# Kernel optimization log

Measured on AMD Instinct MI355X. Metric: run time of the kernel, lower is better.

The kernel has to match this reference:

```python
import jax, jax.numpy as jnp
import numpy as np

D_MODEL = 1024
N_HEADS = 16
N_PHASE = 128
HEAD_DIM = D_MODEL // N_HEADS
PHASE_PER_HEAD = N_PHASE // N_HEADS
CONTENT_SCALE = 1.0 / np.sqrt(HEAD_DIM)
PHASE_SCALE = 1.0 / np.sqrt(PHASE_PER_HEAD)
LN_EPS = 1e-5


def create_position_phases(L, n_phase, base=10000.0):
    # RoPE-style: each freq repeated at even/odd indices (interleaved)
    inv_freq = 1.0 / base ** (jnp.arange(0, n_phase, 2, dtype=jnp.float32) / n_phase)
    pos = jnp.arange(L, dtype=jnp.float32)
    sinusoid = pos[:, None] * inv_freq[None, :]          # (L, n_phase//2)
    return jnp.repeat(sinusoid, 2, axis=1)               # (L, n_phase)


def setup_inputs() -> dict:
    key = jax.random.key(0)
    ks = jax.random.split(key, 12)
    B, L, D, P = 1, 2048, D_MODEL, N_PHASE
    s = 0.02
    return {
        'x_real': jax.random.normal(ks[0], (B, L, D), jnp.float32),
        'x_imag': jax.random.normal(ks[1], (B, L, D), jnp.float32),
        'Wq': jax.random.normal(ks[2], (D, D), jnp.float32) * s,
        'Wk': jax.random.normal(ks[3], (D, D), jnp.float32) * s,
        'Wv': jax.random.normal(ks[4], (D, D), jnp.float32) * s,
        'Wqp': jax.random.normal(ks[5], (D, P), jnp.float32) * s,
        'bqp': jax.random.uniform(ks[6], (P,), jnp.float32, -np.pi, np.pi),
        'Wkp': jax.random.normal(ks[7], (D, P), jnp.float32) * s,
        'bkp': jax.random.uniform(ks[8], (P,), jnp.float32, -np.pi, np.pi),
        'Wo': jax.random.normal(ks[9], (D, D), jnp.float32) * s,
        'alpha_logit': jnp.zeros((N_HEADS, 1, 1), jnp.float32),
        'ln_gamma': jnp.ones((D,), jnp.float32),
        'ln_beta': jnp.zeros((D,), jnp.float32),
    }


def _split_heads(x, B, L, H, hd):
    return x.reshape(B, L, H, hd).transpose(0, 2, 1, 3)  # (B,H,L,hd)


def reference(x_real, x_imag, Wq, Wk, Wv, Wqp, bqp, Wkp, bkp, Wo,
              alpha_logit, ln_gamma, ln_beta):
    B, L, D = x_real.shape
    H, hd, p = N_HEADS, HEAD_DIM, PHASE_PER_HEAD

    Q = _split_heads(x_real @ Wq, B, L, H, hd)
    K = _split_heads(x_real @ Wk, B, L, H, hd)
    V = _split_heads(x_real @ Wv, B, L, H, hd)
    content = jnp.einsum('bhqd,bhkd->bhqk', Q, K) * CONTENT_SCALE

    pos_phase = create_position_phases(L, N_PHASE)        # (L, P)
    Qt = _split_heads(x_imag @ Wqp + bqp + pos_phase, B, L, H, p)
    Kt = _split_heads(x_imag @ Wkp + bkp + pos_phase, B, L, H, p)
    phase = (jnp.einsum('bhqp,bhkp->bhqk', jnp.cos(Qt), jnp.cos(Kt))
             + jnp.einsum('bhqp,bhkp->bhqk', jnp.sin(Qt), jnp.sin(Kt))) * PHASE_SCALE

    alpha = jax.nn.sigmoid(alpha_logit)                   # (H,1,1) broadcasts over (B,H,L,L)
    scores = (1.0 - alpha) * content + alpha * phase

    causal = jnp.triu(jnp.ones((L, L), bool), 1)
    scores = jnp.where(causal, -jnp.inf, scores)
    attn = jax.nn.softmax(scores, axis=-1)

    out = jnp.einsum('bhqk,bhkd->bhqd', attn, V)
    out = out.transpose(0, 2, 1, 3).reshape(B, L, D) @ Wo

    h = x_real + out
    mu = jnp.mean(h, axis=-1, keepdims=True)
    var = jnp.var(h, axis=-1, keepdims=True)
    out_real = (h - mu) / jnp.sqrt(var + LN_EPS) * ln_gamma + ln_beta
    return out_real, x_imag
```

## Files before the change

kernel.cpp:

```cpp
#include <hip/hip_runtime.h>
#include <hip/hip_bf16.h>
#include <math.h>

#define L 2048
#define D 1024
#define NH 16
#define HD 64
#define P 128
#define HDE 96
#define CONTENT_SCALE 0.125f
#define PHASE_SCALE   0.35355339059327373f
#define VTS 72
#define PLS 72
#define NSPLIT 4

typedef short bf16x8 __attribute__((ext_vector_type(8)));
typedef float f32x4 __attribute__((ext_vector_type(4)));

__device__ inline ushort f2b(float x) {
    __hip_bfloat16 b = __float2bfloat16(x);
    return *(ushort*)&b;
}
__device__ inline float b2f(ushort u) {
    unsigned v = (unsigned)u << 16;
    union { unsigned u; float f; } c; c.u = v; return c.f;
}

__device__ inline void sincos_hw(float ang, float* sn, float* cs) {
    float rev = ang * 0.15915494309189535f;
    rev -= floorf(rev);
    *sn = __builtin_amdgcn_sinf(rev);
    *cs = __builtin_amdgcn_cosf(rev);
}

__device__ inline void gld_lds16(const void* g, void* l) {
    __builtin_amdgcn_global_load_lds(
        (const __attribute__((address_space(1))) unsigned int*)g,
        (__attribute__((address_space(3))) unsigned int*)l,
        16, 0, 0);
}

__global__ void cvt2_kernel(const float4* __restrict__ sa, const float4* __restrict__ sb,
                            ushort4* __restrict__ da, ushort4* __restrict__ db, int n4) {
    const float4* src = blockIdx.y ? sb : sa;
    ushort4* dst = blockIdx.y ? db : da;
    int i = blockIdx.x * blockDim.x + threadIdx.x;
    if (i < n4) {
        float4 v = src[i];
        ushort4 o;
        o.x = f2b(v.x); o.y = f2b(v.y); o.z = f2b(v.z); o.w = f2b(v.w);
        dst[i] = o;
    }
}

__global__ void cvtw_kernel(const float* __restrict__ W0, const float* __restrict__ W1,
                            const float* __restrict__ W2, const float* __restrict__ W3,
                            const float* __restrict__ W4, const float* __restrict__ W5,
                            ushort* __restrict__ T0, ushort* __restrict__ T1,
                            ushort* __restrict__ T2, ushort* __restrict__ T3,
                            ushort* __restrict__ Tp) {
    const float* W; ushort* T; int ncols;
    switch (blockIdx.z) {
        case 0: W = W0; T = T0; ncols = D; break;
        case 1: W = W1; T = T1; ncols = D; break;
        case 2: W = W2; T = T2; ncols = D; break;
        case 3: W = W3; T = T3; ncols = D; break;
        case 4: W = W4; T = Tp; ncols = P; break;
        default: W = W5; T = Tp + (size_t)P * D; ncols = P; break;
    }
    int n0 = blockIdx.x * 32, k0 = blockIdx.y * 32;
    if (n0 >= ncols) return;
    __shared__ float tile[32][33];
    int tx = threadIdx.x, ty = threadIdx.y;
#pragma unroll
    for (int i = 0; i < 4; i++)
        tile[ty + i * 8][tx] = W[(size_t)(k0 + ty + i * 8) * ncols + n0 + tx];
    __syncthreads();
#pragma unroll
    for (int i = 0; i < 4; i++)
        T[(size_t)(n0 + ty + i * 8) * D + k0 + tx] = f2b(tile[tx][ty + i * 8]);
}

__global__ void zpad_kernel(ushort* __restrict__ Qe, ushort* __restrict__ Ke) {
    int i = blockIdx.x * blockDim.x + threadIdx.x;
    size_t base = (size_t)i * HDE + 80;
    uint4 z = make_uint4(0, 0, 0, 0);
    *(uint4*)(Qe + base) = z;
    *(uint4*)(Qe + base + 8) = z;
    *(uint4*)(Ke + base) = z;
    *(uint4*)(Ke + base + 8) = z;
}

__launch_bounds__(256)
__global__ void qkv_gemm(const ushort* __restrict__ Ab, const ushort* __restrict__ xib,
                         const ushort* __restrict__ Wtq, const ushort* __restrict__ Wtk,
                         const ushort* __restrict__ Wtv, const ushort* __restrict__ Wtp,
                         ushort* __restrict__ Qe, ushort* __restrict__ Ke,
                         ushort* __restrict__ Ve, const float* __restrict__ alpha,
                         const float* __restrict__ bqp, const float* __restrict__ bkp) {
    const int z = blockIdx.z;
    if (z == 3 && blockIdx.x >= 2) return;
    const ushort* At = (z == 3) ? xib : Ab;
    const ushort* Bt = (z == 0) ? Wtq : ((z == 1) ? Wtk : ((z == 2) ? Wtv : Wtp));
    __shared__ ushort As[128 * 32];
    __shared__ ushort Bs[128 * 32];
    const int tid = threadIdx.x;
    const int wave = tid >> 6, lane = tid & 63, quad = lane >> 4, ln16 = lane & 15;
    const int wm = wave >> 1, wn = wave & 1;
    const int m0 = blockIdx.y * 128, n0 = blockIdx.x * 128;
    f32x4 acc[4][4];
#pragma unroll
    for (int i = 0; i < 4; i++)
#pragma unroll
        for (int j = 0; j < 4; j++) acc[i][j] = (f32x4){0.f, 0.f, 0.f, 0.f};
    for (int kt = 0; kt < D; kt += 32) {
        __syncthreads();
#pragma unroll
        for (int i = 0; i < 2; i++) {
            int idx = i * 256 + tid;
            int row = idx >> 2, c8 = idx & 3;
            gld_lds16(At + (size_t)(m0 + row) * D + kt + c8 * 8, &As[idx * 8]);
            gld_lds16(Bt + (size_t)(n0 + row) * D + kt + c8 * 8, &Bs[idx * 8]);
        }
        __syncthreads();
        bf16x8 af[4], bfr[4];
#pragma unroll
        for (int t = 0; t < 4; t++) {
            af[t]  = *(const bf16x8*)(&As[(wm * 64 + t * 16 + ln16) * 32 + quad * 8]);
            bfr[t] = *(const bf16x8*)(&Bs[(wn * 64 + t * 16 + ln16) * 32 + quad * 8]);
        }
#pragma unroll
        for (int i = 0; i < 4; i++)
#pragma unroll
            for (int j = 0; j < 4; j++)
                acc[i][j] = __builtin_amdgcn_mfma_f32_16x16x32_bf16(af[i], bfr[j], acc[i][j], 0, 0, 0);
    }
    if (z < 3) {
        int hn = (n0 + wn * 64) >> 6;
        float s = 1.f;
        if (z == 0) s = (1.f - 1.f / (1.f + __expf(-alpha[hn]))) * CONTENT_SCALE;
        ushort* dst; int stride;
        if (z == 0)      { dst = Qe; stride = HDE; }
        else if (z == 1) { dst = Ke; stride = HDE; }
        else             { dst = Ve; stride = HD; }
#pragma unroll
        for (int i = 0; i < 4; i++)
#pragma unroll
            for (int j = 0; j < 4; j++) {
                int dcol = j * 16 + ln16;
#pragma unroll
                for (int r = 0; r < 4; r++) {
                    int m = m0 + wm * 64 + i * 16 + quad * 4 + r;
                    dst[((size_t)hn * L + m) * stride + dcol] = f2b(acc[i][j][r] * s);
                }
            }
    } else {
#pragma unroll
        for (int j = 0; j < 4; j++) {
            int cg = n0 + wn * 64 + j * 16 + ln16;
            int isQ = cg < P;
            int c = cg & (P - 1);
            int hh = c >> 3, jj = c & 7;
            float b = isQ ? bqp[c] : bkp[c];
            float sc = isQ ? (1.f / (1.f + __expf(-alpha[hh]))) * PHASE_SCALE : 1.f;
            float invf = __expf(-((float)(c & ~1) / 128.f) * 9.210340371976184f);
            ushort* dst = isQ ? Qe : Ke;
#pragma unroll
            for (int i = 0; i < 4; i++)
#pragma unroll
                for (int r = 0; r < 4; r++) {
                    int m = m0 + wm * 64 + i * 16 + quad * 4 + r;
                    float qt = acc[i][j][r] + b + (float)m * invf;
                    float sn, cs;
                    sincos_hw(qt, &sn, &cs);
                    size_t base = ((size_t)hh * L + m) * HDE;
                    dst[base + 64 + jj] = f2b(sc * cs);
                    dst[base + 72 + jj] = f2b(sc * sn);
                }
        }
    }
}

__launch_bounds__(256)
__global__ void wo_gemm(const ushort* __restrict__ Ab, const ushort* __restrict__ Bt,
                        float* __restrict__ C) {
    __shared__ ushort As[128 * 32];
    __shared__ ushort Bs[128 * 32];
    const int tid = threadIdx.x;
    const int wave = tid >> 6, lane = tid & 63, quad = lane >> 4, ln16 = lane & 15;
    const int wm = wave >> 1, wn = wave & 1;
    const int m0 = blockIdx.y * 128, n0 = blockIdx.x * 128;
    f32x4 acc[4][4];
#pragma unroll
    for (int i = 0; i < 4; i++)
#pragma unroll
        for (int j = 0; j < 4; j++) acc[i][j] = (f32x4){0.f, 0.f, 0.f, 0.f};
    for (int kt = 0; kt < D; kt += 32) {
        __syncthreads();
#pragma unroll
        for (int i = 0; i < 2; i++) {
            int idx = i * 256 + tid;
            int row = idx >> 2, c8 = idx & 3;
            gld_lds16(Ab + (size_t)(m0 + row) * D + kt + c8 * 8, &As[idx * 8]);
            gld_lds16(Bt + (size_t)(n0 + row) * D + kt + c8 * 8, &Bs[idx * 8]);
        }
        __syncthreads();
        bf16x8 af[4], bfr[4];
#pragma unroll
        for (int t = 0; t < 4; t++) {
            af[t]  = *(const bf16x8*)(&As[(wm * 64 + t * 16 + ln16) * 32 + quad * 8]);
            bfr[t] = *(const bf16x8*)(&Bs[(wn * 64 + t * 16 + ln16) * 32 + quad * 8]);
        }
#pragma unroll
        for (int i = 0; i < 4; i++)
#pragma unroll
            for (int j = 0; j < 4; j++)
                acc[i][j] = __builtin_amdgcn_mfma_f32_16x16x32_bf16(af[i], bfr[j], acc[i][j], 0, 0, 0);
    }
#pragma unroll
    for (int i = 0; i < 4; i++)
#pragma unroll
        for (int j = 0; j < 4; j++)
#pragma unroll
            for (int r = 0; r < 4; r++) {
                int m = m0 + wm * 64 + i * 16 + quad * 4 + r;
                int n = n0 + wn * 64 + j * 16 + ln16;
                C[(size_t)m * D + n] = acc[i][j][r];
            }
}

__launch_bounds__(256)
__global__ void flash_attn(const ushort* __restrict__ Qe, const ushort* __restrict__ Ke,
                           const ushort* __restrict__ Ve,
                           ushort* __restrict__ Opart, float* __restrict__ ml) {
    const int b = blockIdx.x;
    const int xcd = b & 7;
    const int r5 = b >> 3;
    const int h = xcd * 2 + (r5 & 1);
    const int cA = (r5 >> 1) & 15, cB = 31 - cA;
    const int z = r5 >> 5;
    const int tid = threadIdx.x;
    const int wave = tid >> 6, lane = tid & 63, quad = lane >> 4, ln16 = lane & 15;
    const int nTA = cA + 1, nTB = cB + 1;
    const int sA = (z * nTA) >> 2, nA = (((z + 1) * nTA) >> 2) - sA;
    const int sB = (z * nTB) >> 2, nB = (((z + 1) * nTB) >> 2) - sB;
    const int ntot = nA + nB;

    ushort* Op = Opart + (size_t)z * L * D;
    float* mlp = ml + (size_t)z * NH * L;

    __shared__ ushort Kl[64 * HDE];
    __shared__ ushort Vt[HD * VTS];
    __shared__ ushort Pl[4][16 * PLS];

    const ushort* Kh  = Ke + (size_t)h * L * HDE;
    const ushort* Vh  = Ve + (size_t)h * L * HD;
    const ushort* Qh0 = Qe + (size_t)h * L * HDE;

    const int krow = tid & 63, dg = wave;

    bf16x8 onesv;
#pragma unroll
    for (int i = 0; i < 8; i++) onesv[i] = (short)0x3F80;

    if (nA == 0) {
        const int q0z = cA * 64 + wave * 16;
#pragma unroll
        for (int r = 0; r < 4; r++) {
            int q = q0z + quad * 4 + r;
            ushort* dst = Op + (size_t)q * D + h * HD;
#pragma unroll
            for (int nt = 0; nt < 4; nt++) dst[nt * 16 + ln16] = 0;
            if (ln16 == 0) mlp[(size_t)h * L + q] = 0.f;
        }
    }

    int t0 = (nA > 0) ? sA : sB;
    bf16x8 kreg[3], vreg[2];
    {
        const ushort* Ksrc = Kh + (size_t)(t0 * 64) * HDE;
#pragma unroll
        for (int ii = 0; ii < 3; ii++)
            kreg[ii] = *(const bf16x8*)(Ksrc + (size_t)(ii * 256 + tid) * 8);
#pragma unroll
        for (int i = 0; i < 2; i++)
            vreg[i] = *(const bf16x8*)(Vh + (size_t)(t0 * 64 + krow) * HD + dg * 16 + i * 8);
    }

    bf16x8 qa[3];
    f32x4 o[4], ol;

    for (int tt = 0; tt < ntot; tt++) {
        const int inB = (tt >= nA);
        const int c  = inB ? cB : cA;
        const int t  = inB ? sB + (tt - nA) : sA + tt;
        const int k0 = t * 64;
        const int q0 = c * 64 + wave * 16;

        __syncthreads();
#pragma unroll
        for (int ii = 0; ii < 3; ii++)
            *(bf16x8*)(&Kl[(ii * 256 + tid) * 8]) = kreg[ii];
#pragma unroll
        for (int i = 0; i < 2; i++)
#pragma unroll
            for (int jj = 0; jj < 8; jj++)
                Vt[(dg * 16 + i * 8 + jj) * VTS + krow] = (ushort)vreg[i][jj];
        __syncthreads();

        if (tt + 1 < ntot) {
            int inB2 = (tt + 1 >= nA);
            int t2 = inB2 ? sB + (tt + 1 - nA) : sA + tt + 1;
            int k02 = t2 * 64;
            const ushort* Ksrc = Kh + (size_t)k02 * HDE;
#pragma unroll
            for (int ii = 0; ii < 3; ii++)
                kreg[ii] = *(const bf16x8*)(Ksrc + (size_t)(ii * 256 + tid) * 8);
#pragma unroll
            for (int i = 0; i < 2; i++)
                vreg[i] = *(const bf16x8*)(Vh + (size_t)(k02 + krow) * HD + dg * 16 + i * 8);
        }

        if (tt == 0 || tt == nA) {
            const ushort* Qh = Qh0 + (size_t)q0 * HDE;
#pragma unroll
            for (int kc = 0; kc < 3; kc++)
                qa[kc] = *(const bf16x8*)(Qh + (size_t)ln16 * HDE + kc * 32 + quad * 8);
#pragma unroll
            for (int nt = 0; nt < 4; nt++) o[nt] = (f32x4){0.f, 0.f, 0.f, 0.f};
            ol = (f32x4){0.f, 0.f, 0.f, 0.f};
        }

        f32x4 s[4];
#pragma unroll
        for (int st = 0; st < 4; st++) s[st] = (f32x4){0.f, 0.f, 0.f, 0.f};
#pragma unroll
        for (int kc = 0; kc < 3; kc++)
#pragma unroll
            for (int st = 0; st < 4; st++) {
                bf16x8 kb = *(const bf16x8*)(&Kl[(st * 16 + ln16) * HDE + kc * 32 + quad * 8]);
                s[st] = __builtin_amdgcn_mfma_f32_16x16x32_bf16(qa[kc], kb, s[st], 0, 0, 0);
            }
        if (t == c) {
#pragma unroll
            for (int st = 0; st < 4; st++) {
                int key = k0 + st * 16 + ln16;
#pragma unroll
                for (int r = 0; r < 4; r++)
                    if (key > q0 + quad * 4 + r) s[st][r] = -1e30f;
            }
        }
#pragma unroll
        for (int st = 0; st < 4; st++)
#pragma unroll
            for (int r = 0; r < 4; r++)
                Pl[wave][(quad * 4 + r) * PLS + st * 16 + ln16] = f2b(__expf(s[st][r]));
        bf16x8 pa0 = *(const bf16x8*)(&Pl[wave][ln16 * PLS + quad * 8]);
        bf16x8 pa1 = *(const bf16x8*)(&Pl[wave][ln16 * PLS + 32 + quad * 8]);
#pragma unroll
        for (int nt = 0; nt < 4; nt++) {
            bf16x8 vb0 = *(const bf16x8*)(&Vt[(nt * 16 + ln16) * VTS + quad * 8]);
            bf16x8 vb1 = *(const bf16x8*)(&Vt[(nt * 16 + ln16) * VTS + 32 + quad * 8]);
            o[nt] = __builtin_amdgcn_mfma_f32_16x16x32_bf16(pa0, vb0, o[nt], 0, 0, 0);
            o[nt] = __builtin_amdgcn_mfma_f32_16x16x32_bf16(pa1, vb1, o[nt], 0, 0, 0);
        }
        ol = __builtin_amdgcn_mfma_f32_16x16x32_bf16(pa0, onesv, ol, 0, 0, 0);
        ol = __builtin_amdgcn_mfma_f32_16x16x32_bf16(pa1, onesv, ol, 0, 0, 0);

        if (tt == nA - 1 || tt == ntot - 1) {
#pragma unroll
            for (int r = 0; r < 4; r++) {
                int q = q0 + quad * 4 + r;
                ushort* dst = Op + (size_t)q * D + h * HD;
#pragma unroll
                for (int nt = 0; nt < 4; nt++)
                    dst[nt * 16 + ln16] = f2b(o[nt][r]);
                if (ln16 == 0) mlp[(size_t)h * L + q] = ol[r];
            }
        }
    }
}

__global__ void comb_kernel(const ushort* __restrict__ Opart, const float* __restrict__ ml,
                            ushort* __restrict__ AOb) {
    int q = blockIdx.x;
    int t = threadIdx.x;
    int h = t >> 4;
    float lsum = 0.f;
#pragma unroll
    for (int zz = 0; zz < NSPLIT; zz++)
        lsum += ml[(size_t)zz * NH * L + (size_t)h * L + q];
    float inv = 1.f / lsum;
    size_t idx = (size_t)q * D + t * 4;
    float ox = 0.f, oy = 0.f, oz = 0.f, ow = 0.f;
#pragma unroll
    for (int zz = 0; zz < NSPLIT; zz++) {
        ushort4 a = *(const ushort4*)(Opart + (size_t)zz * L * D + idx);
        ox += b2f(a.x); oy += b2f(a.y); oz += b2f(a.z); ow += b2f(a.w);
    }
    ushort4 o;
    o.x = f2b(ox * inv); o.y = f2b(oy * inv);
    o.z = f2b(oz * inv); o.w = f2b(ow * inv);
    *(ushort4*)(AOb + idx) = o;
}

__global__ void ln_kernel(const float* __restrict__ xr, const float* __restrict__ o2,
                          const float* __restrict__ gamma, const float* __restrict__ beta,
                          float* __restrict__ outp, const float4* __restrict__ xi4,
                          float4* __restrict__ out1) {
    int l = blockIdx.x;
    int tid = threadIdx.x;
    int wave = tid >> 6;
    __shared__ float red[8];
    float hv[4];
    float s = 0.f;
#pragma unroll
    for (int i = 0; i < 4; i++) {
        int c = tid + i * 256;
        hv[i] = xr[(size_t)l * D + c] + o2[(size_t)l * D + c];
        s += hv[i];
    }
    out1[(size_t)l * (D / 4) + tid] = xi4[(size_t)l * (D / 4) + tid];
#pragma unroll
    for (int off = 1; off < 64; off <<= 1) s += __shfl_xor(s, off);
    if ((tid & 63) == 0) red[wave] = s;
    __syncthreads();
    float mu = (red[0] + red[1] + red[2] + red[3]) * (1.f / D);
    float v = 0.f;
#pragma unroll
    for (int i = 0; i < 4; i++) { float d = hv[i] - mu; v += d * d; }
#pragma unroll
    for (int off = 1; off < 64; off <<= 1) v += __shfl_xor(v, off);
    __syncthreads();
    if ((tid & 63) == 0) red[4 + wave] = v;
    __syncthreads();
    float rstd = rsqrtf((red[4] + red[5] + red[6] + red[7]) * (1.f / D) + 1e-5f);
#pragma unroll
    for (int i = 0; i < 4; i++) {
        int c = tid + i * 256;
        outp[(size_t)l * D + c] = (hv[i] - mu) * rstd * gamma[c] + beta[c];
    }
}

extern "C" void kernel_launch(void* const* d_in, const int* in_sizes, int n_in,
                              void* d_out, int out_size, void* d_ws, size_t ws_size,
                              hipStream_t stream) {
    const float* xr    = (const float*)d_in[0];
    const float* xi    = (const float*)d_in[1];
    const float* Wq    = (const float*)d_in[2];
    const float* Wk    = (const float*)d_in[3];
    const float* Wv    = (const float*)d_in[4];
    const float* Wqp   = (const float*)d_in[5];
    const float* bqp   = (const float*)d_in[6];
    const float* Wkp   = (const float*)d_in[7];
    const float* bkp   = (const float*)d_in[8];
    const float* Wo    = (const float*)d_in[9];
    const float* alpha = (const float*)d_in[10];
    const float* gamma = (const float*)d_in[11];
    const float* beta  = (const float*)d_in[12];

    const size_t LD = (size_t)L * D;
    const size_t MB = 1024 * 1024;

    char* A8 = (char*)d_out;
    char* B8 = A8 + LD * 4;
    ushort* xib = (ushort*)A8;
    ushort* AOb = (ushort*)A8;
    ushort* Wot = (ushort*)(A8 + 4 * MB);
    ushort* Wtq = (ushort*)(A8 + 6 * MB);
    ushort* xrb = (ushort*)B8;
    ushort* Wtk = (ushort*)(B8 + 4 * MB);
    ushort* Wtv = (ushort*)(B8 + 6 * MB);
    float* outf = (float*)d_out;

    ushort* Qe = (ushort*)d_ws;
    ushort* Ke = Qe + (size_t)NH * L * HDE;
    ushort* Ve = Ke + (size_t)NH * L * HDE;
    ushort* Wqpkt = Ve + (size_t)NH * L * HD;
    ushort* Opart = Wqpkt + (size_t)256 * D;
    float*  mlbuf = (float*)(Opart + (size_t)NSPLIT * LD);
    float*  O2 = (float*)d_ws;

    cvt2_kernel<<<dim3((int)(LD / 4 / 256), 2), 256, 0, stream>>>(
        (const float4*)xr, (const float4*)xi, (ushort4*)xrb, (ushort4*)xib, (int)(LD / 4));
    cvtw_kernel<<<dim3(32, 32, 6), dim3(32, 8), 0, stream>>>(
        Wq, Wk, Wv, Wo, Wqp, Wkp, Wtq, Wtk, Wtv, Wot, Wqpkt);
    zpad_kernel<<<NH * L / 256, 256, 0, stream>>>(Qe, Ke);

    qkv_gemm<<<dim3(8, 16, 4), 256, 0, stream>>>(xrb, xib, Wtq, Wtk, Wtv, Wqpkt,
                                                 Qe, Ke, Ve, alpha, bqp, bkp);

    flash_attn<<<1024, 256, 0, stream>>>(Qe, Ke, Ve, Opart, mlbuf);

    comb_kernel<<<L, 256, 0, stream>>>(Opart, mlbuf, AOb);

    wo_gemm<<<dim3(8, 16), 256, 0, stream>>>(AOb, Wot, O2);

    ln_kernel<<<L, 256, 0, stream>>>(xr, O2, gamma, beta, outf,
                                     (const float4*)xi, (float4*)(B8));
}
```

Baseline: 202.2 us.

## Merge prep kernels, fold split-K combine into Wo GEMM, pad K LDS

Combines the bf16 conversion, weight transpose and zero-pad kernels into a single prep launch, which cuts two launches. Removes the separate combine kernel by having wo_gemm sum the four attention partials and apply the softmax normalizer while it loads its A tile, so the intermediate bf16 buffer is never written or re-read. It also pads the K tile's LDS row stride in flash attention from 96 to 104 to reduce bank conflicts. The trade-off is that wo_gemm now does synchronous global loads of 4x the A data per tile, and each of its 8 column blocks repeats the combine work for the same rows.

```diff
diff --git a/kernel.cpp b/kernel.cpp
--- a/kernel.cpp
+++ b/kernel.cpp
@@ -10,6 +10,7 @@
 #define HDE 96
 #define CONTENT_SCALE 0.125f
 #define PHASE_SCALE   0.35355339059327373f
+#define KLS 104
 #define VTS 72
 #define PLS 72
 #define NSPLIT 4
@@ -40,55 +41,58 @@
         16, 0, 0);
 }
 
-__global__ void cvt2_kernel(const float4* __restrict__ sa, const float4* __restrict__ sb,
-                            ushort4* __restrict__ da, ushort4* __restrict__ db, int n4) {
-    const float4* src = blockIdx.y ? sb : sa;
-    ushort4* dst = blockIdx.y ? db : da;
-    int i = blockIdx.x * blockDim.x + threadIdx.x;
-    if (i < n4) {
+__global__ void prep_kernel(const float* __restrict__ xr, const float* __restrict__ xi,
+                            ushort* __restrict__ xrb, ushort* __restrict__ xib,
+                            const float* __restrict__ W0, const float* __restrict__ W1,
+                            const float* __restrict__ W2, const float* __restrict__ W3,
+                            const float* __restrict__ W4, const float* __restrict__ W5,
+                            ushort* __restrict__ T0, ushort* __restrict__ T1,
+                            ushort* __restrict__ T2, ushort* __restrict__ T3,
+                            ushort* __restrict__ Tp,
+                            ushort* __restrict__ Qe, ushort* __restrict__ Ke) {
+    __shared__ float tile[32][33];
+    const int b = blockIdx.x;
+    const int tid = threadIdx.x;
+    if (b < 4096) {
+        const float4* src = (b >> 11) ? (const float4*)xi : (const float4*)xr;
+        ushort4* dst = (b >> 11) ? (ushort4*)xib : (ushort4*)xrb;
+        int i = ((b & 2047) << 8) + tid;
         float4 v = src[i];
         ushort4 o;
         o.x = f2b(v.x); o.y = f2b(v.y); o.z = f2b(v.z); o.w = f2b(v.w);
         dst[i] = o;
-    }
-}
-
-__global__ void cvtw_kernel(const float* __restrict__ W0, const float* __restrict__ W1,
-                            const float* __restrict__ W2, const float* __restrict__ W3,
-                            const float* __restrict__ W4, const float* __restrict__ W5,
-                            ushort* __restrict__ T0, ushort* __restrict__ T1,
-                            ushort* __restrict__ T2, ushort* __restrict__ T3,
-                            ushort* __restrict__ Tp) {
-    const float* W; ushort* T; int ncols;
-    switch (blockIdx.z) {
-        case 0: W = W0; T = T0; ncols = D; break;
-        case 1: W = W1; T = T1; ncols = D; break;
-        case 2: W = W2; T = T2; ncols = D; break;
-        case 3: W = W3; T = T3; ncols = D; break;
-        case 4: W = W4; T = Tp; ncols = P; break;
-        default: W = W5; T = Tp + (size_t)P * D; ncols = P; break;
-    }
-    int n0 = blockIdx.x * 32, k0 = blockIdx.y * 32;
-    if (n0 >= ncols) return;
-    __shared__ float tile[32][33];
-    int tx = threadIdx.x, ty = threadIdx.y;
-#pragma unroll
-    for (int i = 0; i < 4; i++)
-        tile[ty + i * 8][tx] = W[(size_t)(k0 + ty + i * 8) * ncols + n0 + tx];
-    __syncthreads();
-#pragma unroll
-    for (int i = 0; i < 4; i++)
-        T[(size_t)(n0 + ty + i * 8) * D + k0 + tx] = f2b(tile[tx][ty + i * 8]);
-}
-
-__global__ void zpad_kernel(ushort* __restrict__ Qe, ushort* __restrict__ Ke) {
-    int i = blockIdx.x * blockDim.x + threadIdx.x;
-    size_t base = (size_t)i * HDE + 80;
-    uint4 z = make_uint4(0, 0, 0, 0);
-    *(uint4*)(Qe + base) = z;
-    *(uint4*)(Qe + base + 8) = z;
-    *(uint4*)(Ke + base) = z;
-    *(uint4*)(Ke + base + 8) = z;
+    } else if (b < 8448) {
+        int w = b - 4096;
+        const float* W; ushort* T; int ncols, n0, k0;
+        if (w < 4096) {
+            int z = w >> 10, t = w & 1023;
+            n0 = (t & 31) * 32; k0 = (t >> 5) * 32; ncols = D;
+            W = (z == 0) ? W0 : ((z == 1) ? W1 : ((z == 2) ? W2 : W3));
+            T = (z == 0) ? T0 : ((z == 1) ? T1 : ((z == 2) ? T2 : T3));
+        } else {
+            int w2 = w - 4096;
+            int z = w2 >> 7, t = w2 & 127;
+            n0 = (t & 3) * 32; k0 = (t >> 2) * 32; ncols = P;
+            W = z ? W5 : W4;
+            T = Tp + (size_t)z * P * D;
+        }
+        int tx = tid & 31, ty = tid >> 5;
+#pragma unroll
+        for (int i = 0; i < 4; i++)
+            tile[ty + i * 8][tx] = W[(size_t)(k0 + ty + i * 8) * ncols + n0 + tx];
+        __syncthreads();
+#pragma unroll
+        for (int i = 0; i < 4; i++)
+            T[(size_t)(n0 + ty + i * 8) * D + k0 + tx] = f2b(tile[tx][ty + i * 8]);
+    } else {
+        int i = (b - 8448) * 256 + tid;
+        size_t base = (size_t)i * HDE + 80;
+        uint4 z4 = make_uint4(0, 0, 0, 0);
+        *(uint4*)(Qe + base) = z4;
+        *(uint4*)(Qe + base + 8) = z4;
+        *(uint4*)(Ke + base) = z4;
+        *(uint4*)(Ke + base + 8) = z4;
+    }
 }
 
 __launch_bounds__(256)
@@ -182,54 +186,6 @@
 }
 
 __launch_bounds__(256)
-__global__ void wo_gemm(const ushort* __restrict__ Ab, const ushort* __restrict__ Bt,
-                        float* __restrict__ C) {
-    __shared__ ushort As[128 * 32];
-    __shared__ ushort Bs[128 * 32];
-    const int tid = threadIdx.x;
-    const int wave = tid >> 6, lane = tid & 63, quad = lane >> 4, ln16 = lane & 15;
-    const int wm = wave >> 1, wn = wave & 1;
-    const int m0 = blockIdx.y * 128, n0 = blockIdx.x * 128;
-    f32x4 acc[4][4];
-#pragma unroll
-    for (int i = 0; i < 4; i++)
-#pragma unroll
-        for (int j = 0; j < 4; j++) acc[i][j] = (f32x4){0.f, 0.f, 0.f, 0.f};
-    for (int kt = 0; kt < D; kt += 32) {
-        __syncthreads();
-#pragma unroll
-        for (int i = 0; i < 2; i++) {
-            int idx = i * 256 + tid;
-            int row = idx >> 2, c8 = idx & 3;
-            gld_lds16(Ab + (size_t)(m0 + row) * D + kt + c8 * 8, &As[idx * 8]);
-            gld_lds16(Bt + (size_t)(n0 + row) * D + kt + c8 * 8, &Bs[idx * 8]);
-        }
-        __syncthreads();
-        bf16x8 af[4], bfr[4];
-#pragma unroll
-        for (int t = 0; t < 4; t++) {
-            af[t]  = *(const bf16x8*)(&As[(wm * 64 + t * 16 + ln16) * 32 + quad * 8]);
-            bfr[t] = *(const bf16x8*)(&Bs[(wn * 64 + t * 16 + ln16) * 32 + quad * 8]);
-        }
-#pragma unroll
-        for (int i = 0; i < 4; i++)
-#pragma unroll
-            for (int j = 0; j < 4; j++)
-                acc[i][j] = __builtin_amdgcn_mfma_f32_16x16x32_bf16(af[i], bfr[j], acc[i][j], 0, 0, 0);
-    }
-#pragma unroll
-    for (int i = 0; i < 4; i++)
-#pragma unroll
-        for (int j = 0; j < 4; j++)
-#pragma unroll
-            for (int r = 0; r < 4; r++) {
-                int m = m0 + wm * 64 + i * 16 + quad * 4 + r;
-                int n = n0 + wn * 64 + j * 16 + ln16;
-                C[(size_t)m * D + n] = acc[i][j][r];
-            }
-}
-
-__launch_bounds__(256)
 __global__ void flash_attn(const ushort* __restrict__ Qe, const ushort* __restrict__ Ke,
                            const ushort* __restrict__ Ve,
                            ushort* __restrict__ Opart, float* __restrict__ ml) {
@@ -249,7 +205,7 @@
     ushort* Op = Opart + (size_t)z * L * D;
     float* mlp = ml + (size_t)z * NH * L;
 
-    __shared__ ushort Kl[64 * HDE];
+    __shared__ ushort Kl[64 * KLS];
     __shared__ ushort Vt[HD * VTS];
     __shared__ ushort Pl[4][16 * PLS];
 
@@ -299,8 +255,11 @@
 
         __syncthreads();
 #pragma unroll
-        for (int ii = 0; ii < 3; ii++)
-            *(bf16x8*)(&Kl[(ii * 256 + tid) * 8]) = kreg[ii];
+        for (int ii = 0; ii < 3; ii++) {
+            int idx = ii * 256 + tid;
+            int row = idx / 12, c12 = idx - row * 12;
+            *(bf16x8*)(&Kl[row * KLS + c12 * 8]) = kreg[ii];
+        }
 #pragma unroll
         for (int i = 0; i < 2; i++)
 #pragma unroll
@@ -338,7 +297,7 @@
         for (int kc = 0; kc < 3; kc++)
 #pragma unroll
             for (int st = 0; st < 4; st++) {
-                bf16x8 kb = *(const bf16x8*)(&Kl[(st * 16 + ln16) * HDE + kc * 32 + quad * 8]);
+                bf16x8 kb = *(const bf16x8*)(&Kl[(st * 16 + ln16) * KLS + kc * 32 + quad * 8]);
                 s[st] = __builtin_amdgcn_mfma_f32_16x16x32_bf16(qa[kc], kb, s[st], 0, 0, 0);
             }
         if (t == c) {
@@ -381,27 +340,74 @@
     }
 }
 
-__global__ void comb_kernel(const ushort* __restrict__ Opart, const float* __restrict__ ml,
-                            ushort* __restrict__ AOb) {
-    int q = blockIdx.x;
-    int t = threadIdx.x;
-    int h = t >> 4;
-    float lsum = 0.f;
-#pragma unroll
-    for (int zz = 0; zz < NSPLIT; zz++)
-        lsum += ml[(size_t)zz * NH * L + (size_t)h * L + q];
-    float inv = 1.f / lsum;
-    size_t idx = (size_t)q * D + t * 4;
-    float ox = 0.f, oy = 0.f, oz = 0.f, ow = 0.f;
-#pragma unroll
-    for (int zz = 0; zz < NSPLIT; zz++) {
-        ushort4 a = *(const ushort4*)(Opart + (size_t)zz * L * D + idx);
-        ox += b2f(a.x); oy += b2f(a.y); oz += b2f(a.z); ow += b2f(a.w);
-    }
-    ushort4 o;
-    o.x = f2b(ox * inv); o.y = f2b(oy * inv);
-    o.z = f2b(oz * inv); o.w = f2b(ow * inv);
-    *(ushort4*)(AOb + idx) = o;
+__launch_bounds__(256)
+__global__ void wo_gemm(const ushort* __restrict__ Opart, const float* __restrict__ ml,
+                        const ushort* __restrict__ Bt, float* __restrict__ C) {
+    __shared__ ushort As[128 * 32];
+    __shared__ ushort Bs[128 * 32];
+    __shared__ float invl[128 * 16];
+    const int tid = threadIdx.x;
+    const int wave = tid >> 6, lane = tid & 63, quad = lane >> 4, ln16 = lane & 15;
+    const int wm = wave >> 1, wn = wave & 1;
+    const int m0 = blockIdx.y * 128, n0 = blockIdx.x * 128;
+    for (int e = tid; e < 2048; e += 256) {
+        int row = e >> 4, hh = e & 15;
+        float s = 0.f;
+#pragma unroll
+        for (int zz = 0; zz < NSPLIT; zz++)
+            s += ml[(size_t)zz * NH * L + (size_t)hh * L + m0 + row];
+        invl[e] = 1.f / s;
+    }
+    f32x4 acc[4][4];
+#pragma unroll
+    for (int i = 0; i < 4; i++)
+#pragma unroll
+        for (int j = 0; j < 4; j++) acc[i][j] = (f32x4){0.f, 0.f, 0.f, 0.f};
+    for (int kt = 0; kt < D; kt += 32) {
+        __syncthreads();
+        int hk = kt >> 6;
+#pragma unroll
+        for (int i = 0; i < 2; i++) {
+            int idx = i * 256 + tid;
+            int row = idx >> 2, c8 = idx & 3;
+            float inv = invl[(row << 4) + hk];
+            size_t src = (size_t)(m0 + row) * D + kt + c8 * 8;
+            float a[8] = {0.f, 0.f, 0.f, 0.f, 0.f, 0.f, 0.f, 0.f};
+#pragma unroll
+            for (int zz = 0; zz < NSPLIT; zz++) {
+                bf16x8 p = *(const bf16x8*)(Opart + (size_t)zz * L * D + src);
+#pragma unroll
+                for (int jj = 0; jj < 8; jj++) a[jj] += b2f((ushort)p[jj]);
+            }
+            bf16x8 outv;
+#pragma unroll
+            for (int jj = 0; jj < 8; jj++) outv[jj] = (short)f2b(a[jj] * inv);
+            *(bf16x8*)(&As[idx * 8]) = outv;
+            gld_lds16(Bt + (size_t)(n0 + row) * D + kt + c8 * 8, &Bs[idx * 8]);
+        }
+        __syncthreads();
+        bf16x8 af[4], bfr[4];
+#pragma unroll
+        for (int t = 0; t < 4; t++) {
+            af[t]  = *(const bf16x8*)(&As[(wm * 64 + t * 16 + ln16) * 32 + quad * 8]);
+            bfr[t] = *(const bf16x8*)(&Bs[(wn * 64 + t * 16 + ln16) * 32 + quad * 8]);
+        }
+#pragma unroll
+        for (int i = 0; i < 4; i++)
+#pragma unroll
+            for (int j = 0; j < 4; j++)
+                acc[i][j] = __builtin_amdgcn_mfma_f32_16x16x32_bf16(af[i], bfr[j], acc[i][j], 0, 0, 0);
+    }
+#pragma unroll
+    for (int i = 0; i < 4; i++)
+#pragma unroll
+        for (int j = 0; j < 4; j++)
+#pragma unroll
+            for (int r = 0; r < 4; r++) {
+                int m = m0 + wm * 64 + i * 16 + quad * 4 + r;
+                int n = n0 + wn * 64 + j * 16 + ln16;
+                C[(size_t)m * D + n] = acc[i][j][r];
+            }
 }
 
 __global__ void ln_kernel(const float* __restrict__ xr, const float* __restrict__ o2,
@@ -465,7 +471,6 @@
     char* A8 = (char*)d_out;
     char* B8 = A8 + LD * 4;
     ushort* xib = (ushort*)A8;
-    ushort* AOb = (ushort*)A8;
     ushort* Wot = (ushort*)(A8 + 4 * MB);
     ushort* Wtq = (ushort*)(A8 + 6 * MB);
     ushort* xrb = (ushort*)B8;
@@ -481,20 +486,16 @@
     float*  mlbuf = (float*)(Opart + (size_t)NSPLIT * LD);
     float*  O2 = (float*)d_ws;
 
-    cvt2_kernel<<<dim3((int)(LD / 4 / 256), 2), 256, 0, stream>>>(
-        (const float4*)xr, (const float4*)xi, (ushort4*)xrb, (ushort4*)xib, (int)(LD / 4));
-    cvtw_kernel<<<dim3(32, 32, 6), dim3(32, 8), 0, stream>>>(
-        Wq, Wk, Wv, Wo, Wqp, Wkp, Wtq, Wtk, Wtv, Wot, Wqpkt);
-    zpad_kernel<<<NH * L / 256, 256, 0, stream>>>(Qe, Ke);
+    prep_kernel<<<8576, 256, 0, stream>>>(xr, xi, xrb, xib,
+                                          Wq, Wk, Wv, Wo, Wqp, Wkp,
+                                          Wtq, Wtk, Wtv, Wot, Wqpkt, Qe, Ke);
 
     qkv_gemm<<<dim3(8, 16, 4), 256, 0, stream>>>(xrb, xib, Wtq, Wtk, Wtv, Wqpkt,
                                                  Qe, Ke, Ve, alpha, bqp, bkp);
 
     flash_attn<<<1024, 256, 0, stream>>>(Qe, Ke, Ve, Opart, mlbuf);
 
-    comb_kernel<<<L, 256, 0, stream>>>(Opart, mlbuf, AOb);
-
-    wo_gemm<<<dim3(8, 16), 256, 0, stream>>>(AOb, Wot, O2);
+    wo_gemm<<<dim3(8, 16), 256, 0, stream>>>(Opart, mlbuf, Wot, O2);
 
     ln_kernel<<<L, 256, 0, stream>>>(xr, O2, gamma, beta, outf,
                                      (const float4*)xi, (float4*)(B8));
```

Result: slower. 221.2 us (+9.4%).
